# Optimization experiments

Hardware: AMD Instinct MI355X
Metric: run time of the kernel (lower is better)

The kernel has to match this reference:

```python
import jax, jax.numpy as jnp
import numpy as np

EPS = 1e-05

def setup_inputs() -> dict:
    key = jax.random.key(0)
    k1, = jax.random.split(key, 1)
    x = jax.random.normal(k1, (4, 4096, 2048), dtype=jnp.float32)
    g = jnp.ones((2048,), dtype=jnp.float32)
    return {"x": x, "g": g}

def reference(x, g):
    # RMSNorm: x / sqrt(mean(x^2, axis=-1) + eps) * g, computed in fp32
    dtype = x.dtype
    xf = x.astype(jnp.float32)
    ms = jnp.mean(xf * xf, axis=-1, keepdims=True)  # [B,S,1]
    out = xf * jax.lax.rsqrt(ms + EPS) * g
    return out.astype(dtype)
```

## Files before the change

### kernel.cpp

```cpp
#include <hip/hip_runtime.h>
#include <stdint.h>

#define ROW_LEN 2048
#define R4      512
#define BLOCK   256
#define NR      8
#define EPS     1e-5f

typedef __attribute__((address_space(1))) unsigned int u32_g;
typedef __attribute__((address_space(3))) unsigned int u32_l;

__device__ __forceinline__ void gload_lds16(const float4* src, float4* lds_dst) {
    __builtin_amdgcn_global_load_lds((const u32_g*)(const void*)src,
                                     (u32_l*)(void*)lds_dst, 16, 0, 0);
}

__global__ __launch_bounds__(BLOCK) void RMSNorm_56607668961691_kernel(
    const float* __restrict__ x,
    const float* __restrict__ g,
    float* __restrict__ out)
{
    __shared__ float4 lds[2][BLOCK / 64][R4];

    const int wave = threadIdx.x >> 6;
    const int lane = threadIdx.x & 63;
    const size_t wid  = (size_t)blockIdx.x * (BLOCK / 64) + wave;
    const size_t row0 = wid * NR;

    const float4* __restrict__ xr   = reinterpret_cast<const float4*>(x) + row0 * R4 + lane;
    float4* __restrict__       outr = reinterpret_cast<float4*>(out)     + row0 * R4 + lane;
    const float4* __restrict__ gv   = reinterpret_cast<const float4*>(g) + lane;

    #pragma unroll
    for (int j = 0; j < 8; ++j)
        gload_lds16(xr + j * 64, &lds[0][wave][j * 64]);

    float4 gr[8];
    #pragma unroll
    for (int j = 0; j < 8; ++j) gr[j] = gv[j * 64];

    #pragma unroll 1
    for (int r = 0; r < NR; ++r) {
        const int cur = r & 1;

        asm volatile("s_waitcnt vmcnt(8)" ::: "memory");

        float4 v[8];
        #pragma unroll
        for (int j = 0; j < 8; ++j) v[j] = lds[cur][wave][j * 64 + lane];

        __builtin_amdgcn_sched_barrier(0);

        if (r + 1 < NR) {
            const float4* xn = xr + (size_t)(r + 1) * R4;
            #pragma unroll
            for (int j = 0; j < 8; ++j)
                gload_lds16(xn + j * 64, &lds[cur ^ 1][wave][j * 64]);
        }

        float s0 = 0.f, s1 = 0.f, s2 = 0.f, s3 = 0.f;
        #pragma unroll
        for (int j = 0; j < 8; ++j) {
            s0 += v[j].x * v[j].x;
            s1 += v[j].y * v[j].y;
            s2 += v[j].z * v[j].z;
            s3 += v[j].w * v[j].w;
        }
        float ss = (s0 + s1) + (s2 + s3);

        #pragma unroll
        for (int off = 32; off > 0; off >>= 1)
            ss += __shfl_xor(ss, off, 64);

        const float scale = rsqrtf(ss * (1.0f / (float)ROW_LEN) + EPS);

        float4* o = outr + (size_t)r * R4;
        #pragma unroll
        for (int j = 0; j < 8; ++j) {
            float4 ov;
            ov.x = v[j].x * scale * gr[j].x;
            ov.y = v[j].y * scale * gr[j].y;
            ov.z = v[j].z * scale * gr[j].z;
            ov.w = v[j].w * scale * gr[j].w;
            o[j * 64] = ov;
        }
    }
}

extern "C" void kernel_launch(void* const* d_in, const int* in_sizes, int n_in,
                              void* d_out, int out_size, void* d_ws, size_t ws_size,
                              hipStream_t stream) {
    const float* x = (const float*)d_in[0];
    const float* g = (const float*)d_in[1];
    float* out = (float*)d_out;

    const int rows = in_sizes[0] / ROW_LEN;
    const int grid = rows / ((BLOCK / 64) * NR);
    RMSNorm_56607668961691_kernel<<<grid, BLOCK, 0, stream>>>(x, g, out);
}
```

Measured before the change: 238.9 us.

## Triple-buffer LDS row prefetch with two-row lookahead and unrolled row loop

Result: no change. 236.8 us (-0.9%).

```diff
diff --git a/kernel.cpp b/kernel.cpp
--- a/kernel.cpp
+++ b/kernel.cpp
@@ -1,9 +1,9 @@
 #include <hip/hip_runtime.h>
-#include <stdint.h>
 
 #define ROW_LEN 2048
 #define R4      512
 #define BLOCK   256
+#define WAVES   (BLOCK / 64)
 #define NR      8
 #define EPS     1e-5f
 
@@ -15,48 +15,56 @@
                                      (u32_l*)(void*)lds_dst, 16, 0, 0);
 }
 
+template<int N>
+__device__ __forceinline__ void wait_vm() {
+    asm volatile("s_waitcnt vmcnt(%0)" :: "n"(N) : "memory");
+    __builtin_amdgcn_sched_barrier(0);
+}
+
 __global__ __launch_bounds__(BLOCK) void RMSNorm_56607668961691_kernel(
     const float* __restrict__ x,
     const float* __restrict__ g,
     float* __restrict__ out)
 {
-    __shared__ float4 lds[2][BLOCK / 64][R4];
+    __shared__ float4 lds[3][WAVES][R4];
 
     const int wave = threadIdx.x >> 6;
     const int lane = threadIdx.x & 63;
-    const size_t wid  = (size_t)blockIdx.x * (BLOCK / 64) + wave;
+    const size_t wid  = (size_t)blockIdx.x * WAVES + wave;
     const size_t row0 = wid * NR;
 
-    const float4* __restrict__ xr   = reinterpret_cast<const float4*>(x) + row0 * R4 + lane;
-    float4* __restrict__       outr = reinterpret_cast<float4*>(out)     + row0 * R4 + lane;
-    const float4* __restrict__ gv   = reinterpret_cast<const float4*>(g) + lane;
-
-    #pragma unroll
-    for (int j = 0; j < 8; ++j)
-        gload_lds16(xr + j * 64, &lds[0][wave][j * 64]);
+    const float4* xr   = reinterpret_cast<const float4*>(x)   + row0 * R4 + lane;
+    float4*       outr = reinterpret_cast<float4*>(out)       + row0 * R4 + lane;
+    const float4* gv   = reinterpret_cast<const float4*>(g)   + lane;
 
     float4 gr[8];
     #pragma unroll
     for (int j = 0; j < 8; ++j) gr[j] = gv[j * 64];
 
-    #pragma unroll 1
+    #pragma unroll
+    for (int j = 0; j < 8; ++j) gload_lds16(xr + j * 64,      &lds[0][wave][j * 64]);
+    #pragma unroll
+    for (int j = 0; j < 8; ++j) gload_lds16(xr + R4 + j * 64, &lds[1][wave][j * 64]);
+
+    #pragma unroll
     for (int r = 0; r < NR; ++r) {
-        const int cur = r & 1;
+        if (r + 2 < NR) {
+            const float4* xn = xr + (size_t)(r + 2) * R4;
+            float4* dst = &lds[(r + 2) % 3][wave][0];
+            #pragma unroll
+            for (int j = 0; j < 8; ++j) gload_lds16(xn + j * 64, dst + j * 64);
+        }
 
-        asm volatile("s_waitcnt vmcnt(8)" ::: "memory");
+        if      (r == 0)      wait_vm<16>();
+        else if (r == 1)      wait_vm<24>();
+        else if (r <  NR - 2) wait_vm<32>();
+        else if (r == NR - 2) wait_vm<24>();
+        else                  wait_vm<16>();
 
+        const float4* b = &lds[r % 3][wave][0];
         float4 v[8];
         #pragma unroll
-        for (int j = 0; j < 8; ++j) v[j] = lds[cur][wave][j * 64 + lane];
-
-        __builtin_amdgcn_sched_barrier(0);
-
-        if (r + 1 < NR) {
-            const float4* xn = xr + (size_t)(r + 1) * R4;
-            #pragma unroll
-            for (int j = 0; j < 8; ++j)
-                gload_lds16(xn + j * 64, &lds[cur ^ 1][wave][j * 64]);
-        }
+        for (int j = 0; j < 8; ++j) v[j] = b[j * 64 + lane];
 
         float s0 = 0.f, s1 = 0.f, s2 = 0.f, s3 = 0.f;
         #pragma unroll
@@ -84,6 +92,9 @@
             ov.w = v[j].w * scale * gr[j].w;
             o[j * 64] = ov;
         }
+
+        asm volatile("" ::: "memory");
+        __builtin_amdgcn_sched_barrier(0);
     }
 }
 
@@ -95,6 +106,6 @@
     float* out = (float*)d_out;
 
     const int rows = in_sizes[0] / ROW_LEN;
-    const int grid = rows / ((BLOCK / 64) * NR);
+    const int grid = rows / (WAVES * NR);
     RMSNorm_56607668961691_kernel<<<grid, BLOCK, 0, stream>>>(x, g, out);
 }
```
